# Kernel tuning notes

Measured on AMD Instinct MI355X. Metric: run time of the kernel, lower is better.

The kernel has to match this reference:

```python
import jax, jax.numpy as jnp
import numpy as np

V = 50257   # vocab size (output_size / num_words)
H = 500     # hidden_size
S = 256     # source sequence length
MAXLEN = 64 # greedy decode steps
SOS = 1


def _gru_scan(xs, Wih, Whh, bih, bhh, reverse=False):
    """Run a GRU over xs: (S, Din) -> (outputs (S,H), final hidden (H,)).
    PyTorch gate order: r, z, n."""
    gx = xs @ Wih.T + bih  # (S, 3H), input-side gates precomputed
    Hh = Whh.shape[1]
    h0 = jnp.zeros((Hh,), dtype=xs.dtype)

    def step(h, g):
        gh = Whh @ h + bhh
        rx, zx, nx = jnp.split(g, 3)
        rh, zh, nh = jnp.split(gh, 3)
        r = jax.nn.sigmoid(rx + rh)
        z = jax.nn.sigmoid(zx + zh)
        n = jnp.tanh(nx + r * nh)
        h2 = (1.0 - z) * n + z * h
        return h2, h2

    hT, ys = jax.lax.scan(step, h0, gx, reverse=reverse)
    return ys, hT


def _gru_cell(x, h, Wih, Whh, bih, bhh):
    gx = Wih @ x + bih
    gh = Whh @ h + bhh
    rx, zx, nx = jnp.split(gx, 3)
    rh, zh, nh = jnp.split(gh, 3)
    r = jax.nn.sigmoid(rx + rh)
    z = jax.nn.sigmoid(zx + zh)
    n = jnp.tanh(nx + r * nh)
    return (1.0 - z) * n + z * h


def setup_inputs() -> dict:
    key = jax.random.key(0)
    ks = jax.random.split(key, 32)

    def p(k, shape):
        return jax.random.normal(k, shape, dtype=jnp.float32) * 0.05

    inp = {}
    inp["input_seq"] = jax.random.randint(ks[0], (S, 1), 0, V)
    inp["input_length"] = S
    inp["max_length"] = MAXLEN
    inp["emb"] = p(ks[1], (V, H))
    i = 2
    for name, din in [("enc0f", H), ("enc0b", H), ("enc1f", 2 * H), ("enc1b", 2 * H)]:
        inp[name + "_Wih"] = p(ks[i], (3 * H, din)); i += 1
        inp[name + "_Whh"] = p(ks[i], (3 * H, H)); i += 1
        inp[name + "_bih"] = p(ks[i], (3 * H,)); i += 1
        inp[name + "_bhh"] = p(ks[i], (3 * H,)); i += 1
    inp["dec_Wih"] = p(ks[i], (2, 3 * H, H)); i += 1
    inp["dec_Whh"] = p(ks[i], (2, 3 * H, H)); i += 1
    inp["dec_bih"] = p(ks[i], (2, 3 * H)); i += 1
    inp["dec_bhh"] = p(ks[i], (2, 3 * H)); i += 1
    inp["concat_W"] = p(ks[i], (H, 2 * H)); i += 1
    inp["concat_b"] = p(ks[i], (H,)); i += 1
    inp["out_W"] = p(ks[i], (V, H)); i += 1
    inp["out_b"] = p(ks[i], (V,)); i += 1
    return inp


def reference(input_seq, input_length, max_length, emb,
              enc0f_Wih, enc0f_Whh, enc0f_bih, enc0f_bhh,
              enc0b_Wih, enc0b_Whh, enc0b_bih, enc0b_bhh,
              enc1f_Wih, enc1f_Whh, enc1f_bih, enc1f_bhh,
              enc1b_Wih, enc1b_Whh, enc1b_bih, enc1b_bhh,
              dec_Wih, dec_Whh, dec_bih, dec_bhh,
              concat_W, concat_b, out_W, out_b):
    tokens = input_seq[:, 0]  # batch = 1
    ex = emb[tokens]          # (S, H) embedding lookup (dropout is eval no-op)

    # --- bidirectional 2-layer encoder GRU (full-length seq, batch=1) ---
    y0f, h0f = _gru_scan(ex, enc0f_Wih, enc0f_Whh, enc0f_bih, enc0f_bhh)
    y0b, h0b = _gru_scan(ex, enc0b_Wih, enc0b_Whh, enc0b_bih, enc0b_bhh, reverse=True)
    x1 = jnp.concatenate([y0f, y0b], axis=1)  # (S, 2H)
    y1f, _ = _gru_scan(x1, enc1f_Wih, enc1f_Whh, enc1f_bih, enc1f_bhh)
    y1b, _ = _gru_scan(x1, enc1b_Wih, enc1b_Whh, enc1b_bih, enc1b_bhh, reverse=True)
    enc_out = y1f + y1b  # (S, H): outputs[:, :H] + outputs[:, H:]

    # encoder_hidden[:n_layers] = [layer0_fwd, layer0_bwd] (PyTorch ordering)
    h_dec0 = jnp.stack([h0f, h0b])  # (2, H)

    def step(carry, _):
        h, tok = carry
        x = emb[tok]  # (H,)
        hs = []
        for l in range(2):  # 2 decoder GRU layers (dropout off in eval)
            hl = _gru_cell(x, h[l], dec_Wih[l], dec_Whh[l], dec_bih[l], dec_bhh[l])
            hs.append(hl)
            x = hl
        h2 = jnp.stack(hs)
        rnn = x  # (H,) top-layer output
        scores = enc_out @ rnn                 # dot attention: (S,)
        w = jax.nn.softmax(scores)
        ctx = w @ enc_out                      # (H,)
        c = jnp.tanh(concat_W @ jnp.concatenate([rnn, ctx]) + concat_b)
        probs = jax.nn.softmax(out_W @ c + out_b)  # (V,)
        tok2 = jnp.argmax(probs).astype(jnp.int32)
        return (h2, tok2), (tok2, probs)

    init = (h_dec0, jnp.asarray(SOS, dtype=jnp.int32))
    _, (all_tokens, all_probs) = jax.lax.scan(step, init, None, length=int(max_length))
    return all_tokens, all_probs
```

## Files before the change

### kernel.cpp

```cpp
#include <hip/hip_runtime.h>
#include <math.h>

typedef unsigned long long ull;

constexpr int H    = 500;
constexpr int H3   = 1500;
constexpr int SEQ  = 256;
constexpr int V    = 50257;
constexpr int TDEC = 64;
constexpr int NLT  = (V + 255) / 256;
constexpr int SB   = 50;
constexpr int UPB  = 10;
constexpr int NDB  = 256;
constexpr int VPB  = (V + NDB - 1) / NDB;
constexpr int WB   = 32;

__device__ __forceinline__ float sigmoidf_(float x) { return 1.f / (1.f + expf(-x)); }

__device__ __forceinline__ float wred(float v) {
  #pragma unroll
  for (int off = 32; off > 0; off >>= 1) v += __shfl_down(v, off, 64);
  return v;
}

__device__ __forceinline__ float gload(const float* p) {
  return __hip_atomic_load((float*)p, __ATOMIC_RELAXED, __HIP_MEMORY_SCOPE_AGENT);
}
__device__ __forceinline__ void gstore(float* p, float v) {
  __hip_atomic_store(p, v, __ATOMIC_RELAXED, __HIP_MEMORY_SCOPE_AGENT);
}
__device__ __forceinline__ int gload_i(const int* p) {
  return __hip_atomic_load((int*)p, __ATOMIC_RELAXED, __HIP_MEMORY_SCOPE_AGENT);
}
__device__ __forceinline__ ull gload64(const ull* p) {
  return __hip_atomic_load((ull*)p, __ATOMIC_RELAXED, __HIP_MEMORY_SCOPE_AGENT);
}
__device__ __forceinline__ void gstore64(ull* p, ull v) {
  __hip_atomic_store(p, v, __ATOMIC_RELAXED, __HIP_MEMORY_SCOPE_AGENT);
}

template<int N, int SLP>
__device__ __forceinline__ void poll_tags(const ull* tags, unsigned want,
                                          float* dst, int tid) {
  constexpr int NW = (N + 63) / 64;
  if (tid < 64) {
    ull v[NW];
    bool ok;
    do {
      ok = true;
      #pragma unroll
      for (int j = 0; j < NW; ++j) {
        int k = tid + (j << 6);
        if (k < N) {
          v[j] = gload64(&tags[k]);
          if ((unsigned)(v[j] >> 32) != want) ok = false;
        }
      }
      if (!ok) __builtin_amdgcn_s_sleep(SLP);
    } while (!ok);
    #pragma unroll
    for (int j = 0; j < NW; ++j) {
      int k = tid + (j << 6);
      if (k < N) dst[k] = __uint_as_float((unsigned)v[j]);
    }
  }
  __syncthreads();
}

__global__ void init_k(ull* ttok) {
  if (threadIdx.x == 0) ttok[0] = (1ull << 32) | 1ull;
}

__global__ void embed_k(const int* __restrict__ seq, const float* __restrict__ emb,
                        float* __restrict__ ex) {
  int t = blockIdx.x;
  int tok = seq[t];
  for (int i = threadIdx.x; i < H; i += blockDim.x)
    ex[(size_t)t * H + i] = emb[(size_t)tok * H + i];
}

__global__ __launch_bounds__(256) void gemm_nt(const float* __restrict__ X,
                                               const float* __restrict__ W,
                                               const float* __restrict__ bias,
                                               float* __restrict__ C,
                                               int M, int N, int K) {
  __shared__ float Xs[64][17];
  __shared__ float Ws[64][17];
  int bm = blockIdx.y * 64, bn = blockIdx.x * 64;
  int tid = threadIdx.x;
  int tx = tid % 16, ty = tid / 16;
  float acc[4][4] = {};
  for (int k0 = 0; k0 < K; k0 += 16) {
    for (int i = tid; i < 64 * 16; i += 256) {
      int m = i / 16, k = i % 16;
      int gm = bm + m, gk = k0 + k, gn = bn + m;
      Xs[m][k] = (gm < M && gk < K) ? X[(size_t)gm * K + gk] : 0.f;
      Ws[m][k] = (gn < N && gk < K) ? W[(size_t)gn * K + gk] : 0.f;
    }
    __syncthreads();
    #pragma unroll
    for (int k = 0; k < 16; ++k) {
      float xv[4], wv[4];
      #pragma unroll
      for (int i = 0; i < 4; ++i) xv[i] = Xs[ty * 4 + i][k];
      #pragma unroll
      for (int j = 0; j < 4; ++j) wv[j] = Ws[tx * 4 + j][k];
      #pragma unroll
      for (int i = 0; i < 4; ++i)
        #pragma unroll
        for (int j = 0; j < 4; ++j) acc[i][j] += xv[i] * wv[j];
    }
    __syncthreads();
  }
  for (int i = 0; i < 4; ++i) {
    int gm = bm + ty * 4 + i;
    if (gm >= M) continue;
    for (int j = 0; j < 4; ++j) {
      int gn = bn + tx * 4 + j;
      if (gn >= N) continue;
      C[(size_t)gm * N + gn] = acc[i][j] + bias[gn];
    }
  }
}

__global__ __launch_bounds__(512, 1) void gru_scan_tag(
    const float* __restrict__ gxF, const float* __restrict__ gxB,
    const float* __restrict__ WhhF, const float* __restrict__ WhhB,
    const float* __restrict__ bhhF, const float* __restrict__ bhhB,
    ull* __restrict__ tAF, ull* __restrict__ tBF,
    ull* __restrict__ tAB, ull* __restrict__ tBB,
    float* __restrict__ yF, float* __restrict__ yB, int ystride) {
  __shared__ float gates[32];
  __shared__ float h_lds[512];
  int dir = blockIdx.x / SB;
  int bu  = blockIdx.x % SB;
  int u0  = bu * UPB;
  const float* gx  = dir ? gxB : gxF;
  const float* Whh = dir ? WhhB : WhhF;
  const float* bhh = dir ? bhhB : bhhF;
  ull* tagA = dir ? tAB : tAF;
  ull* tagB = dir ? tBB : tBF;
  float* y  = dir ? yB : yF;
  int tid = threadIdx.x, lane = tid & 63, wid = tid >> 6;

  float wreg[4][8];
  #pragma unroll
  for (int rr = 0; rr < 4; ++rr) {
    int r = wid + 8 * rr;
    #pragma unroll
    for (int j = 0; j < 8; ++j) {
      int k = lane + 64 * j;
      wreg[rr][j] = (r < 30 && k < 500)
          ? Whh[(size_t)((r / UPB) * 500 + u0 + (r % UPB)) * 500 + k] : 0.f;
    }
  }
  int u = u0 + tid;
  float br = 0.f, bz = 0.f, bn = 0.f;
  if (tid < UPB) { br = bhh[u]; bz = bhh[500 + u]; bn = bhh[1000 + u]; }
  h_lds[tid] = 0.f;
  __syncthreads();

  for (int t = 0; t < SEQ; ++t) {
    ull* wout = (t & 1) ? tagA : tagB;
    ull* win  = (t & 1) ? tagB : tagA;
    int teff = dir ? (SEQ - 1 - t) : t;

    float gxr = 0.f, gxz = 0.f, gxn = 0.f;
    if (tid < UPB) {
      const float* g = gx + (size_t)teff * H3;
      gxr = g[u]; gxz = g[500 + u]; gxn = g[1000 + u];
    }

    if (t > 0 && wid == 0) {
      ull v[8];
      for (;;) {
        bool ok = true;
        #pragma unroll
        for (int j = 0; j < 8; ++j) {
          int k = lane + 64 * j;
          if (k < 500) {
            v[j] = gload64(&win[k]);
            if ((unsigned)(v[j] >> 32) != (unsigned)t) ok = false;
          }
        }
        if (ok) break;
        __builtin_amdgcn_s_sleep(1);
      }
      #pragma unroll
      for (int j = 0; j < 8; ++j) {
        int k = lane + 64 * j;
        if (k < 500) h_lds[k] = __uint_as_float((unsigned)v[j]);
      }
    }
    __syncthreads();

    float hold = (tid < UPB) ? h_lds[u] : 0.f;
    float hreg[8];
    #pragma unroll
    for (int j = 0; j < 8; ++j) {
      int k = lane + 64 * j;
      hreg[j] = (k < 500) ? h_lds[k] : 0.f;
    }
    #pragma unroll
    for (int rr = 0; rr < 4; ++rr) {
      int r = wid + 8 * rr;
      if (r < 30) {
        float acc = 0.f;
        #pragma unroll
        for (int j = 0; j < 8; ++j) acc += wreg[rr][j] * hreg[j];
        acc = wred(acc);
        if (lane == 0) gates[r] = acc;
      }
    }
    __syncthreads();
    if (tid < UPB) {
      float rr = sigmoidf_(gxr + gates[tid]           + br);
      float zz = sigmoidf_(gxz + gates[UPB + tid]     + bz);
      float nn = tanhf(    gxn + rr * (gates[2 * UPB + tid] + bn));
      float hp = (1.f - zz) * nn + zz * hold;
      ull pv = ((ull)(unsigned)(t + 1) << 32) | (ull)__float_as_uint(hp);
      gstore64(&wout[u], pv);
      y[(size_t)teff * ystride + u] = hp;
    }
  }
}

__global__ void seed_k(const ull* __restrict__ tf, const ull* __restrict__ tb,
                       ull* __restrict__ th0a, ull* __restrict__ th1a) {
  int i = threadIdx.x;
  if (i < 500) {
    th0a[i] = (ull)(unsigned)tf[i];
    th1a[i] = (ull)(unsigned)tb[i];
  }
}

__global__ void add_k(const float* __restrict__ a, const float* __restrict__ b,
                      float* __restrict__ c, int n) {
  int i = blockIdx.x * blockDim.x + threadIdx.x;
  if (i < n) c[i] = a[i] + b[i];
}

__global__ __launch_bounds__(256) void transposeE_k(const float* __restrict__ A,
                                                    float* __restrict__ B) {
  __shared__ float t[64][65];
  int c0 = blockIdx.x * 64;
  int r0 = blockIdx.y * 64;
  int tx = threadIdx.x & 63, ty = threadIdx.x >> 6;
  #pragma unroll
  for (int i = 0; i < 64; i += 4) {
    int r = r0 + ty + i, c = c0 + tx;
    if (r < SEQ && c < 500) t[ty + i][tx] = A[(size_t)r * 500 + c];
  }
  __syncthreads();
  #pragma unroll
  for (int i = 0; i < 64; i += 4) {
    int c = c0 + ty + i, r = r0 + tx;
    if (c < 500 && r < SEQ) B[(size_t)c * SEQ + r] = t[tx][ty + i];
  }
}

__device__ __forceinline__ void cell_unit_tag(int u, int lane,
    const float* xf, const float* hf,
    const float* __restrict__ Wih, const float* __restrict__ Whh,
    const float* __restrict__ bih, const float* __restrict__ bhh,
    ull* htag, unsigned want) {
  float g[6];
  #pragma unroll
  for (int kind = 0; kind < 6; ++kind) {
    const float* row = (kind < 3) ? (Wih + (size_t)(kind * 500 + u) * 500)
                                  : (Whh + (size_t)((kind - 3) * 500 + u) * 500);
    const float* vec = (kind < 3) ? xf : hf;
    float acc = 0.f;
    #pragma unroll
    for (int j = 0; j < 8; ++j) {
      int k = lane + 64 * j;
      if (k < 500) acc += row[k] * vec[k];
    }
    g[kind] = wred(acc);
  }
  if (lane == 0) {
    float r = sigmoidf_(g[0] + bih[u]        + g[3] + bhh[u]);
    float z = sigmoidf_(g[1] + bih[500 + u]  + g[4] + bhh[500 + u]);
    float n = tanhf(    g[2] + bih[1000 + u] + r * (g[5] + bhh[1000 + u]));
    float hv = (1.f - z) * n + z * hf[u];
    gstore64(&htag[u], ((ull)want << 32) | (ull)__float_as_uint(hv));
  }
}

__global__ __launch_bounds__(1024, 4) void dec_persist(
    const float* __restrict__ emb,
    const float* __restrict__ dWih, const float* __restrict__ dWhh,
    const float* __restrict__ dbih, const float* __restrict__ dbhh,
    const float* __restrict__ enc_out, const float* __restrict__ enc_outT,
    const float* __restrict__ cW, const float* __restrict__ cb,
    const float* __restrict__ outW, const float* __restrict__ outb,
    ull* __restrict__ th0a, ull* __restrict__ th0b,
    ull* __restrict__ th1a, ull* __restrict__ th1b,
    ull* __restrict__ tsc, ull* __restrict__ tctx, ull* __restrict__ tcvec,
    ull* __restrict__ ttok,
    float* __restrict__ lg0, float* __restrict__ lg1,
    float* __restrict__ pm, float* __restrict__ ps, int* __restrict__ pix,
    float* __restrict__ stats, float* __restrict__ out_tokens,
    float* __restrict__ out_probs, int* __restrict__ dcnt) {
  __shared__ float4 v4[250];
  __shared__ float hfull[512];
  __shared__ float red[256], sc[256];
  __shared__ float wm[16], wsum[16]; __shared__ int wix[16];
  __shared__ float mm[256], ms[256]; __shared__ int mi[256];
  __shared__ int lastf, sh_tk;
  float* xf = (float*)v4;
  float* hf = xf + 500;
  int tid = threadIdx.x, lane = tid & 63, wid = tid >> 6, blk = blockIdx.x;
  bool worker = blk < WB;
  int u = blk * 16 + wid;

  for (int st = 0; st < TDEC; ++st) {
    unsigned want = (unsigned)(st + 1);
    ull* h0r = (st & 1) ? th0b : th0a;
    ull* h0w = (st & 1) ? th0a : th0b;
    ull* h1r = (st & 1) ? th1b : th1a;
    ull* h1w = (st & 1) ? th1a : th1b;
    float* lg_w = (st & 1) ? lg1 : lg0;
    const float* lg_r = (st & 1) ? lg0 : lg1;

    if (worker) {
      if (tid == 0) {
        ull tv;
        for (;;) {
          tv = gload64(ttok);
          if ((unsigned)(tv >> 32) == want) break;
          __builtin_amdgcn_s_sleep(1);
        }
        sh_tk = (int)(unsigned)tv;
      }
      __syncthreads();
      int tk = sh_tk;
      if (tid >= 64) {
        for (int i = tid - 64; i < 500; i += 960) xf[i] = emb[(size_t)tk * 500 + i];
      } else {
        #pragma unroll
        for (int j = 0; j < 8; ++j) {
          int k = tid + (j << 6);
          if (k < 500) hf[k] = __uint_as_float((unsigned)gload64(&h0r[k]));
        }
      }
      __syncthreads();
      if (u < 500) cell_unit_tag(u, lane, xf, hf, dWih, dWhh, dbih, dbhh, h0w, want);
      __syncthreads();

      if (tid >= 64) {
        for (int i = tid - 64; i < 500; i += 960)
          hf[i] = __uint_as_float((unsigned)gload64(&h1r[i]));
      }
      poll_tags<500, 1>(h0w, want, xf, tid);
      if (u < 500) cell_unit_tag(u, lane, xf, hf,
          dWih + 750000, dWhh + 750000, dbih + 1500, dbhh + 1500, h1w, want);

      poll_tags<500, 1>(h1w, want, hfull, tid);
      if (wid < 8) {
        int s = blk * 8 + wid;
        const float* row = enc_out + (size_t)s * 500;
        float acc = 0.f;
        #pragma unroll
        for (int j = 0; j < 8; ++j) {
          int k = lane + 64 * j;
          if (k < 500) acc += row[k] * hfull[k];
        }
        acc = wred(acc);
        if (lane == 0) gstore64(&tsc[s], ((ull)want << 32) | (ull)__float_as_uint(acc));
      }
      poll_tags<256, 1>(tsc, want, sc, tid);

      {
        float myv = (tid < 256) ? sc[tid] : 0.f;
        if (tid < 256) red[tid] = myv;
        __syncthreads();
        for (int s = 128; s > 0; s >>= 1) {
          if (tid < s) red[tid] = fmaxf(red[tid], red[tid + s]);
          __syncthreads();
        }
        float m = red[0]; __syncthreads();
        float e = 0.f;
        if (tid < 256) { e = expf(myv - m); red[tid] = e; }
        __syncthreads();
        for (int s = 128; s > 0; s >>= 1) {
          if (tid < s) red[tid] += red[tid + s];
          __syncthreads();
        }
        float inv = 1.f / red[0]; __syncthreads();
        if (tid < 256) sc[tid] = e * inv;
        __syncthreads();
        int j = blk * 16 + wid;
        if (j < 500) {
          const float* col = enc_outT + (size_t)j * SEQ;
          float acc = 0.f;
          #pragma unroll
          for (int q = 0; q < 4; ++q) {
            int s = lane + 64 * q;
            acc += sc[s] * col[s];
          }
          acc = wred(acc);
          if (lane == 0) gstore64(&tctx[j], ((ull)want << 32) | (ull)__float_as_uint(acc));
        }
      }

      if (tid >= 64) for (int i = tid - 64; i < 500; i += 960) xf[i] = hfull[i];
      poll_tags<500, 1>(tctx, want, hf, tid);
      {
        int i = blk * 16 + wid;
        if (i < 500) {
          const float* row = cW + (size_t)i * 1000;
          float acc = 0.f;
          #pragma unroll
          for (int j = 0; j < 16; ++j) {
            int k = lane + 64 * j;
            if (k < 1000) acc += row[k] * xf[k];
          }
          acc = wred(acc);
          if (lane == 0)
            gstore64(&tcvec[i], ((ull)want << 32) | (ull)__float_as_uint(tanhf(acc + cb[i])));
        }
      }
      __syncthreads();
    } else {
      if (tid == 0) {
        while ((unsigned)(gload64(ttok) >> 32) < want) __builtin_amdgcn_s_sleep(2);
      }
      __syncthreads();
      if (st > 0) {
        float mM = gload(&stats[2 * (st - 1)]), iS = gload(&stats[2 * (st - 1) + 1]);
        int base = blk * VPB;
        for (int r = tid; r < VPB; r += 1024) {
          int v = base + r;
          if (v < V) out_probs[(size_t)(st - 1) * V + v] = expf(lg_r[v] - mM) * iS;
        }
      }
    }

    if (worker) poll_tags<500, 1>(tcvec, want, xf, tid);
    else        poll_tags<500, 4>(tcvec, want, xf, tid);
    const float4* c4 = v4;
    {
      int lstart = wid * 13, lend = lstart + 13;
      if (lstart > VPB) lstart = VPB;
      if (lend > VPB) lend = VPB;
      int r0 = blk * VPB + lstart, r1 = blk * VPB + lend; if (r1 > V) r1 = V;
      float m = -1e30f, ssum = 0.f; int ix = V;
      for (int rb = r0; rb < r1; rb += 8) {
        int nr = r1 - rb; if (nr > 8) nr = 8;
        float a[8] = {0.f, 0.f, 0.f, 0.f, 0.f, 0.f, 0.f, 0.f};
        #pragma unroll
        for (int q = 0; q < 2; ++q) {
          int k4 = lane + 64 * q;
          if (k4 < 125) {
            float4 cc = c4[k4];
            #pragma unroll
            for (int rr = 0; rr < 8; ++rr) {
              if (rr < nr) {
                float4 w4 = ((const float4*)(outW + (size_t)(rb + rr) * 500))[k4];
                a[rr] += w4.x * cc.x + w4.y * cc.y + w4.z * cc.z + w4.w * cc.w;
              }
            }
          }
        }
        #pragma unroll
        for (int rr = 0; rr < 8; ++rr) {
          if (rr < nr) {
            float l = wred(a[rr]);
            if (lane == 0) {
              l += outb[rb + rr];
              lg_w[rb + rr] = l;
              if (l > m) { ssum = ssum * expf(m - l) + 1.f; m = l; ix = rb + rr; }
              else       { ssum += expf(l - m); }
            }
          }
        }
      }
      if (lane == 0) { wm[wid] = m; wsum[wid] = ssum; wix[wid] = ix; }
    }
    __syncthreads();
    if (tid == 0) {
      float M = wm[0], S = wsum[0]; int I = wix[0];
      for (int w2 = 1; w2 < 16; ++w2) {
        if (wm[w2] > M) { S = S * expf(M - wm[w2]) + wsum[w2]; M = wm[w2]; I = wix[w2]; }
        else            { S += wsum[w2] * expf(wm[w2] - M); }
      }
      gstore(&pm[blk], M); gstore(&ps[blk], S);
      __hip_atomic_store(&pix[blk], I, __ATOMIC_RELAXED, __HIP_MEMORY_SCOPE_AGENT);
      __builtin_amdgcn_s_waitcnt(0);
      int prev = __hip_atomic_fetch_add(&dcnt[st], 1, __ATOMIC_RELAXED,
                                        __HIP_MEMORY_SCOPE_AGENT);
      lastf = (prev == NDB - 1) ? 1 : 0;
    }
    __syncthreads();

    if (lastf) {
      if (tid < 256) { mm[tid] = gload(&pm[tid]); ms[tid] = gload(&ps[tid]); mi[tid] = gload_i(&pix[tid]); }
      __syncthreads();
      for (int s = 128; s > 0; s >>= 1) {
        if (tid < s) {
          float ma = mm[tid], mb = mm[tid + s];
          float sa = ms[tid], sb = ms[tid + s];
          int ia = mi[tid], ib = mi[tid + s];
          if (mb > ma || (mb == ma && ib < ia)) {
            ms[tid] = sa * expf(ma - mb) + sb; mm[tid] = mb; mi[tid] = ib;
          } else {
            ms[tid] = sa + sb * expf(mb - ma);
          }
        }
        __syncthreads();
      }
      if (tid == 0) {
        out_tokens[st] = (float)mi[0];
        gstore(&stats[2 * st], mm[0]);
        gstore(&stats[2 * st + 1], 1.f / ms[0]);
        __builtin_amdgcn_s_waitcnt(0);
        gstore64(ttok, ((ull)(unsigned)(st + 2) << 32) | (ull)(unsigned)mi[0]);
      }
    }

    if (worker && st > 0) {
      float mM = gload(&stats[2 * (st - 1)]), iS = gload(&stats[2 * (st - 1) + 1]);
      int base = blk * VPB;
      for (int r = tid; r < VPB; r += 1024) {
        int v = base + r;
        if (v < V) out_probs[(size_t)(st - 1) * V + v] = expf(lg_r[v] - mM) * iS;
      }
    }
    __syncthreads();
  }
}

__global__ __launch_bounds__(256) void probs_k(const float* __restrict__ logits,
    const float* __restrict__ stats, float* __restrict__ out_probs) {
  int v = blockIdx.x * 256 + threadIdx.x;
  if (v < V) out_probs[v] = expf(logits[v] - stats[0]) * stats[1];
}

extern "C" void kernel_launch(void* const* d_in, const int* in_sizes, int n_in,
                              void* d_out, int out_size, void* d_ws, size_t ws_size,
                              hipStream_t stream) {
  const int*   seq   = (const int*)d_in[0];
  const float* emb   = (const float*)d_in[3];
  const float* e0f_Wih = (const float*)d_in[4];
  const float* e0f_Whh = (const float*)d_in[5];
  const float* e0f_bih = (const float*)d_in[6];
  const float* e0f_bhh = (const float*)d_in[7];
  const float* e0b_Wih = (const float*)d_in[8];
  const float* e0b_Whh = (const float*)d_in[9];
  const float* e0b_bih = (const float*)d_in[10];
  const float* e0b_bhh = (const float*)d_in[11];
  const float* e1f_Wih = (const float*)d_in[12];
  const float* e1f_Whh = (const float*)d_in[13];
  const float* e1f_bih = (const float*)d_in[14];
  const float* e1f_bhh = (const float*)d_in[15];
  const float* e1b_Wih = (const float*)d_in[16];
  const float* e1b_Whh = (const float*)d_in[17];
  const float* e1b_bih = (const float*)d_in[18];
  const float* e1b_bhh = (const float*)d_in[19];
  const float* dWih = (const float*)d_in[20];
  const float* dWhh = (const float*)d_in[21];
  const float* dbih = (const float*)d_in[22];
  const float* dbhh = (const float*)d_in[23];
  const float* cW   = (const float*)d_in[24];
  const float* cb   = (const float*)d_in[25];
  const float* outW = (const float*)d_in[26];
  const float* outb = (const float*)d_in[27];

  float* w = (float*)d_ws;
  float* ex      = w;
  float* x1      = ex + 128000;
  float* gxf     = x1 + 256000;
  float* gxb     = gxf + 384000;
  float* y1f     = gxb + 384000;
  float* y1b     = y1f + 128000;
  float* enc_out = y1b + 128000;
  float* lg0     = enc_out + 128000;
  float* lg1     = lg0 + 50432;
  float* pm      = lg1 + 50432;
  float* ps      = pm + 256;
  float* stats   = ps + 256;
  int*   pix     = (int*)(stats + 192);
  int*   dcnt    = pix + 256;
  ull*   htag    = (ull*)(dcnt + 64);
  ull* tL0F_A = htag;        ull* tL0F_B = htag + 512;
  ull* tL0B_A = htag + 1024; ull* tL0B_B = htag + 1536;
  ull* tL1F_A = htag + 2048; ull* tL1F_B = htag + 2560;
  ull* tL1B_A = htag + 3072; ull* tL1B_B = htag + 3584;
  ull*   dtag    = htag + 4096;
  ull* th0a  = dtag;        ull* th0b = dtag + 512;
  ull* th1a  = dtag + 1024; ull* th1b = dtag + 1536;
  ull* tsc   = dtag + 2048; ull* tctx = dtag + 2304;
  ull* tcvec = dtag + 2816; ull* ttok = dtag + 3328;
  float* enc_outT = (float*)(dtag + 3400);

  float* outf = (float*)d_out;

  (void)hipMemsetAsync(dcnt, 0, 64 * sizeof(int) + 7488 * sizeof(ull), stream);

  init_k<<<1, 64, 0, stream>>>(ttok);
  embed_k<<<SEQ, 128, 0, stream>>>(seq, emb, ex);

  gemm_nt<<<dim3(24, 4), 256, 0, stream>>>(ex, e0f_Wih, e0f_bih, gxf, SEQ, H3, H);
  gemm_nt<<<dim3(24, 4), 256, 0, stream>>>(ex, e0b_Wih, e0b_bih, gxb, SEQ, H3, H);
  gru_scan_tag<<<2 * SB, 512, 0, stream>>>(gxf, gxb, e0f_Whh, e0b_Whh,
      e0f_bhh, e0b_bhh, tL0F_A, tL0F_B, tL0B_A, tL0B_B, x1, x1 + 500, 1000);

  gemm_nt<<<dim3(24, 4), 256, 0, stream>>>(x1, e1f_Wih, e1f_bih, gxf, SEQ, H3, 2 * H);
  gemm_nt<<<dim3(24, 4), 256, 0, stream>>>(x1, e1b_Wih, e1b_bih, gxb, SEQ, H3, 2 * H);
  gru_scan_tag<<<2 * SB, 512, 0, stream>>>(gxf, gxb, e1f_Whh, e1b_Whh,
      e1f_bhh, e1b_bhh, tL1F_A, tL1F_B, tL1B_A, tL1B_B, y1f, y1b, 500);
  add_k<<<(SEQ * H + 255) / 256, 256, 0, stream>>>(y1f, y1b, enc_out, SEQ * H);
  transposeE_k<<<dim3(8, 4), 256, 0, stream>>>(enc_out, enc_outT);

  seed_k<<<1, 512, 0, stream>>>(tL0F_A, tL0B_A, th0a, th1a);

  dec_persist<<<NDB, 1024, 0, stream>>>(emb,
      dWih, dWhh, dbih, dbhh, enc_out, enc_outT, cW, cb, outW, outb,
      th0a, th0b, th1a, th1b, tsc, tctx, tcvec, ttok,
      lg0, lg1, pm, ps, pix, stats, outf, outf + TDEC, dcnt);

  probs_k<<<NLT, 256, 0, stream>>>(((TDEC - 1) & 1) ? lg1 : lg0,
      stats + 2 * (TDEC - 1), outf + TDEC + (size_t)(TDEC - 1) * V);
}
```

Measured before the change: 6.665 ms.

## Repartition persistent decoder into 512 blocks of 512 threads with split attention polling

The persistent decoder grid moves from 256 blocks of 1024 threads to 512 blocks of 512 threads. The number of worker blocks grows to 63, so GRU units, context and concat rows are spread over more blocks at 8 warps each. Only the first 32 blocks compute attention scores, while the other workers poll the hidden and score tags together in a new combined poll. The output-projection loop now preloads all outW float4s into registers before doing the FMAs, to increase memory-level parallelism. The cross-block reduction buffers are resized to 512. This raises register pressure and puts more spinning blocks on the global tag flags.

```diff
diff --git a/kernel.cpp b/kernel.cpp
--- a/kernel.cpp
+++ b/kernel.cpp
@@ -11,9 +11,9 @@
 constexpr int NLT  = (V + 255) / 256;
 constexpr int SB   = 50;
 constexpr int UPB  = 10;
-constexpr int NDB  = 256;
+constexpr int NDB  = 512;
 constexpr int VPB  = (V + NDB - 1) / NDB;
-constexpr int WB   = 32;
+constexpr int WB   = 63;
 
 __device__ __forceinline__ float sigmoidf_(float x) { return 1.f / (1.f + expf(-x)); }
 
@@ -62,6 +62,44 @@
     for (int j = 0; j < NW; ++j) {
       int k = tid + (j << 6);
       if (k < N) dst[k] = __uint_as_float((unsigned)v[j]);
+    }
+  }
+  __syncthreads();
+}
+
+__device__ __forceinline__ void poll2_tags(const ull* tA, float* dA,
+                                           const ull* tB, float* dB,
+                                           unsigned want, int tid) {
+  if (tid < 64) {
+    ull va[8], vb[4];
+    bool ok;
+    do {
+      ok = true;
+      #pragma unroll
+      for (int j = 0; j < 8; ++j) {
+        int k = tid + (j << 6);
+        if (k < 500) {
+          va[j] = gload64(&tA[k]);
+          if ((unsigned)(va[j] >> 32) != want) ok = false;
+        }
+      }
+      #pragma unroll
+      for (int j = 0; j < 4; ++j) {
+        int k = tid + (j << 6);
+        vb[j] = gload64(&tB[k]);
+        if ((unsigned)(vb[j] >> 32) != want) ok = false;
+      }
+      if (!ok) __builtin_amdgcn_s_sleep(1);
+    } while (!ok);
+    #pragma unroll
+    for (int j = 0; j < 8; ++j) {
+      int k = tid + (j << 6);
+      if (k < 500) dA[k] = __uint_as_float((unsigned)va[j]);
+    }
+    #pragma unroll
+    for (int j = 0; j < 4; ++j) {
+      int k = tid + (j << 6);
+      dB[k] = __uint_as_float((unsigned)vb[j]);
     }
   }
   __syncthreads();
@@ -287,7 +325,7 @@
   }
 }
 
-__global__ __launch_bounds__(1024, 4) void dec_persist(
+__global__ __launch_bounds__(512, 4) void dec_persist(
     const float* __restrict__ emb,
     const float* __restrict__ dWih, const float* __restrict__ dWhh,
     const float* __restrict__ dbih, const float* __restrict__ dbhh,
@@ -305,14 +343,14 @@
   __shared__ float4 v4[250];
   __shared__ float hfull[512];
   __shared__ float red[256], sc[256];
-  __shared__ float wm[16], wsum[16]; __shared__ int wix[16];
-  __shared__ float mm[256], ms[256]; __shared__ int mi[256];
+  __shared__ float wm[8], wsum[8]; __shared__ int wix[8];
+  __shared__ float mm[512], ms[512]; __shared__ int mi[512];
   __shared__ int lastf, sh_tk;
   float* xf = (float*)v4;
   float* hf = xf + 500;
   int tid = threadIdx.x, lane = tid & 63, wid = tid >> 6, blk = blockIdx.x;
   bool worker = blk < WB;
-  int u = blk * 16 + wid;
+  int u = blk * 8 + wid;
 
   for (int st = 0; st < TDEC; ++st) {
     unsigned want = (unsigned)(st + 1);
@@ -336,7 +374,7 @@
       __syncthreads();
       int tk = sh_tk;
       if (tid >= 64) {
-        for (int i = tid - 64; i < 500; i += 960) xf[i] = emb[(size_t)tk * 500 + i];
+        for (int i = tid - 64; i < 500; i += 448) xf[i] = emb[(size_t)tk * 500 + i];
       } else {
         #pragma unroll
         for (int j = 0; j < 8; ++j) {
@@ -349,15 +387,16 @@
       __syncthreads();
 
       if (tid >= 64) {
-        for (int i = tid - 64; i < 500; i += 960)
+        for (int i = tid - 64; i < 500; i += 448)
           hf[i] = __uint_as_float((unsigned)gload64(&h1r[i]));
       }
       poll_tags<500, 1>(h0w, want, xf, tid);
       if (u < 500) cell_unit_tag(u, lane, xf, hf,
           dWih + 750000, dWhh + 750000, dbih + 1500, dbhh + 1500, h1w, want);
-
-      poll_tags<500, 1>(h1w, want, hfull, tid);
-      if (wid < 8) {
+      __syncthreads();
+
+      if (blk < 32) {
+        poll_tags<500, 1>(h1w, want, hfull, tid);
         int s = blk * 8 + wid;
         const float* row = enc_out + (size_t)s * 500;
         float acc = 0.f;
@@ -368,8 +407,10 @@
         }
         acc = wred(acc);
         if (lane == 0) gstore64(&tsc[s], ((ull)want << 32) | (ull)__float_as_uint(acc));
-      }
-      poll_tags<256, 1>(tsc, want, sc, tid);
+        poll_tags<256, 1>(tsc, want, sc, tid);
+      } else {
+        poll2_tags(h1w, hfull, tsc, sc, want, tid);
+      }
 
       {
         float myv = (tid < 256) ? sc[tid] : 0.f;
@@ -390,7 +431,7 @@
         float inv = 1.f / red[0]; __syncthreads();
         if (tid < 256) sc[tid] = e * inv;
         __syncthreads();
-        int j = blk * 16 + wid;
+        int j = blk * 8 + wid;
         if (j < 500) {
           const float* col = enc_outT + (size_t)j * SEQ;
           float acc = 0.f;
@@ -404,10 +445,10 @@
         }
       }
 
-      if (tid >= 64) for (int i = tid - 64; i < 500; i += 960) xf[i] = hfull[i];
+      if (tid >= 64) for (int i = tid - 64; i < 500; i += 448) xf[i] = hfull[i];
       poll_tags<500, 1>(tctx, want, hf, tid);
       {
-        int i = blk * 16 + wid;
+        int i = blk * 8 + wid;
         if (i < 500) {
           const float* row = cW + (size_t)i * 1000;
           float acc = 0.f;
@@ -430,7 +471,7 @@
       if (st > 0) {
         float mM = gload(&stats[2 * (st - 1)]), iS = gload(&stats[2 * (st - 1) + 1]);
         int base = blk * VPB;
-        for (int r = tid; r < VPB; r += 1024) {
+        for (int r = tid; r < VPB; r += 512) {
           int v = base + r;
           if (v < V) out_probs[(size_t)(st - 1) * V + v] = expf(lg_r[v] - mM) * iS;
         }
@@ -448,18 +489,40 @@
       float m = -1e30f, ssum = 0.f; int ix = V;
       for (int rb = r0; rb < r1; rb += 8) {
         int nr = r1 - rb; if (nr > 8) nr = 8;
-        float a[8] = {0.f, 0.f, 0.f, 0.f, 0.f, 0.f, 0.f, 0.f};
-        #pragma unroll
-        for (int q = 0; q < 2; ++q) {
-          int k4 = lane + 64 * q;
-          if (k4 < 125) {
-            float4 cc = c4[k4];
-            #pragma unroll
-            for (int rr = 0; rr < 8; ++rr) {
-              if (rr < nr) {
-                float4 w4 = ((const float4*)(outW + (size_t)(rb + rr) * 500))[k4];
-                a[rr] += w4.x * cc.x + w4.y * cc.y + w4.z * cc.z + w4.w * cc.w;
-              }
+        float4 wv0[8], wv1[8];
+        #pragma unroll
+        for (int rr = 0; rr < 8; ++rr) {
+          wv0[rr] = (lane < 125 && rr < nr)
+              ? ((const float4*)(outW + (size_t)(rb + rr) * 500))[lane]
+              : make_float4(0.f, 0.f, 0.f, 0.f);
+        }
+        #pragma unroll
+        for (int rr = 0; rr < 8; ++rr) {
+          int k4 = lane + 64;
+          wv1[rr] = (k4 < 125 && rr < nr)
+              ? ((const float4*)(outW + (size_t)(rb + rr) * 500))[k4]
+              : make_float4(0.f, 0.f, 0.f, 0.f);
+        }
+        float a[8];
+        #pragma unroll
+        for (int rr = 0; rr < 8; ++rr) a[rr] = 0.f;
+        if (lane < 125) {
+          float4 cc = c4[lane];
+          #pragma unroll
+          for (int rr = 0; rr < 8; ++rr) {
+            if (rr < nr) {
+              float4 w4 = wv0[rr];
+              a[rr] += w4.x * cc.x + w4.y * cc.y + w4.z * cc.z + w4.w * cc.w;
+            }
+          }
+        }
+        if (lane + 64 < 125) {
+          float4 cc = c4[lane + 64];
+          #pragma unroll
+          for (int rr = 0; rr < 8; ++rr) {
+            if (rr < nr) {
+              float4 w4 = wv1[rr];
+              a[rr] += w4.x * cc.x + w4.y * cc.y + w4.z * cc.z + w4.w * cc.w;
             }
           }
         }
@@ -481,7 +544,7 @@
     __syncthreads();
     if (tid == 0) {
       float M = wm[0], S = wsum[0]; int I = wix[0];
-      for (int w2 = 1; w2 < 16; ++w2) {
+      for (int w2 = 1; w2 < 8; ++w2) {
         if (wm[w2] > M) { S = S * expf(M - wm[w2]) + wsum[w2]; M = wm[w2]; I = wix[w2]; }
         else            { S += wsum[w2] * expf(wm[w2] - M); }
       }
@@ -495,9 +558,9 @@
     __syncthreads();
 
     if (lastf) {
-      if (tid < 256) { mm[tid] = gload(&pm[tid]); ms[tid] = gload(&ps[tid]); mi[tid] = gload_i(&pix[tid]); }
+      { mm[tid] = gload(&pm[tid]); ms[tid] = gload(&ps[tid]); mi[tid] = gload_i(&pix[tid]); }
       __syncthreads();
-      for (int s = 128; s > 0; s >>= 1) {
+      for (int s = 256; s > 0; s >>= 1) {
         if (tid < s) {
           float ma = mm[tid], mb = mm[tid + s];
           float sa = ms[tid], sb = ms[tid + s];
@@ -522,7 +585,7 @@
     if (worker && st > 0) {
       float mM = gload(&stats[2 * (st - 1)]), iS = gload(&stats[2 * (st - 1) + 1]);
       int base = blk * VPB;
-      for (int r = tid; r < VPB; r += 1024) {
+      for (int r = tid; r < VPB; r += 512) {
         int v = base + r;
         if (v < V) out_probs[(size_t)(st - 1) * V + v] = expf(lg_r[v] - mM) * iS;
       }
@@ -578,10 +641,10 @@
   float* lg0     = enc_out + 128000;
   float* lg1     = lg0 + 50432;
   float* pm      = lg1 + 50432;
-  float* ps      = pm + 256;
-  float* stats   = ps + 256;
+  float* ps      = pm + 512;
+  float* stats   = ps + 512;
   int*   pix     = (int*)(stats + 192);
-  int*   dcnt    = pix + 256;
+  int*   dcnt    = pix + 512;
   ull*   htag    = (ull*)(dcnt + 64);
   ull* tL0F_A = htag;        ull* tL0F_B = htag + 512;
   ull* tL0B_A = htag + 1024; ull* tL0B_B = htag + 1536;
@@ -615,7 +678,7 @@
 
   seed_k<<<1, 512, 0, stream>>>(tL0F_A, tL0B_A, th0a, th1a);
 
-  dec_persist<<<NDB, 1024, 0, stream>>>(emb,
+  dec_persist<<<NDB, 512, 0, stream>>>(emb,
       dWih, dWhh, dbih, dbhh, enc_out, enc_outT, cW, cb, outW, outb,
       th0a, th0b, th1a, th1b, tsc, tctx, tcvec, ttok,
       lg0, lg1, pm, ps, pix, stats, outf, outf + TDEC, dcnt);
```

Result: no change. 6.786 ms (+1.8%).
